# Kernel tuning notes

Measured on AMD Instinct MI355X. Metric: run time of the kernel, lower is better.

Reference implementation:

```python
import jax, jax.numpy as jnp
import numpy as np

C = 256
R = 2
HEADS = 8
HEAD_DIM = C // HEADS
SCALE = HEAD_DIM ** -0.5
EPS = 1e-5


def setup_inputs() -> dict:
    key = jax.random.key(0)
    ks = jax.random.split(key, 7)
    x = jax.random.normal(ks[0], (8, C, 64, 64), dtype=jnp.float32)
    # qkv 1x1 conv weight [3C, C], no bias
    w_qkv = jax.random.normal(ks[1], (3 * C, C), dtype=jnp.float32) * (C ** -0.5)
    # depthwise ConvTranspose2d(C, C, k=r, stride=r, groups=C): weight [C, r, r], bias [C]
    w_lp = jax.random.normal(ks[2], (C, R, R), dtype=jnp.float32) * 0.5
    b_lp = jax.random.normal(ks[3], (C,), dtype=jnp.float32) * 0.01
    # GroupNorm(1, C) affine params
    gamma = jnp.ones((C,), dtype=jnp.float32)
    beta = jnp.zeros((C,), dtype=jnp.float32)
    # proj 1x1 conv weight [C, C], no bias
    w_proj = jax.random.normal(ks[4], (C, C), dtype=jnp.float32) * (C ** -0.5)
    return {"x": x, "w_qkv": w_qkv, "w_lp": w_lp, "b_lp": b_lp,
            "gamma": gamma, "beta": beta, "w_proj": w_proj}


def reference(x, w_qkv, w_lp, b_lp, gamma, beta, w_proj):
    # sparse_sampler: AvgPool2d(kernel=1, stride=r) == strided subsampling
    xs = x[:, :, ::R, ::R]                      # [B, C, H, W]
    B, _, H, W = xs.shape
    N = H * W
    # qkv 1x1 conv -> [B, 3C, N] -> [B, heads, 3*head_dim, N]
    qkv = jnp.einsum('oc,bcn->bon', w_qkv, xs.reshape(B, C, N))
    qkv = qkv.reshape(B, HEADS, 3 * HEAD_DIM, N)
    q, k, v = jnp.split(qkv, 3, axis=2)         # each [B, h, d, N]
    # attn[b,h,i,j] = softmax_j( (q^T k)[i,j] * scale )
    attn = jax.nn.softmax(jnp.einsum('bhdi,bhdj->bhij', q, k) * SCALE, axis=-1)
    # out[b,h,d,i] = sum_j v[b,h,d,j] attn[b,h,i,j]
    out = jnp.einsum('bhdj,bhij->bhdi', v, attn).reshape(B, C, H, W)
    # depthwise ConvTranspose2d kernel=r stride=r (non-overlapping): broadcast each
    # pixel into an r x r block weighted by the per-channel kernel, plus bias.
    up = jnp.einsum('bchw,cpq->bchpwq', out, w_lp).reshape(B, C, H * R, W * R)
    up = up + b_lp[None, :, None, None]
    # GroupNorm with 1 group: normalize over (C, H, W) per sample
    mu = jnp.mean(up, axis=(1, 2, 3), keepdims=True)
    var = jnp.var(up, axis=(1, 2, 3), keepdims=True)
    normed = (up - mu) * jax.lax.rsqrt(var + EPS)
    normed = normed * gamma[None, :, None, None] + beta[None, :, None, None]
    # proj 1x1 conv
    Bo, _, Ho, Wo = normed.shape
    y = jnp.einsum('oc,bcn->bon', w_proj, normed.reshape(Bo, C, Ho * Wo))
    return y.reshape(Bo, C, Ho, Wo)
```

## Files before the change

kernel.cpp:

```cpp
#include <hip/hip_runtime.h>
#include <hip/hip_bf16.h>

#define ATT_SCALE_L2E 0.2550322540f

typedef __attribute__((ext_vector_type(8))) short bf16x8;
typedef __attribute__((ext_vector_type(4))) short bf16x4;
typedef __attribute__((ext_vector_type(4))) float f32x4;
typedef __attribute__((ext_vector_type(16))) float f32x16;
typedef __attribute__((ext_vector_type(4))) int i32x4;

#define MFMA16(a, b, c) __builtin_amdgcn_mfma_f32_16x16x32_bf16(a, b, c, 0, 0, 0)
#define MFMA32(a, b, c) __builtin_amdgcn_mfma_f32_32x32x16_bf16(a, b, c, 0, 0, 0)

__device__ inline short f2b(float f) {
    return __builtin_bit_cast(short, __float2bfloat16(f));
}

__device__ inline bf16x8 cat4(bf16x4 a, bf16x4 b) {
    bf16x8 r;
    r[0] = a[0]; r[1] = a[1]; r[2] = a[2]; r[3] = a[3];
    r[4] = b[0]; r[5] = b[1]; r[6] = b[2]; r[7] = b[3];
    return r;
}

__device__ inline int cvt_pk(float a, float b) {
    int r;
    asm("v_cvt_pk_bf16_f32 %0, %1, %2" : "=v"(r) : "v"(a), "v"(b));
    return r;
}

__global__ __launch_bounds__(256) void wconv_k(const float* __restrict__ w,
                                               short* __restrict__ wb) {
    int i0 = (blockIdx.x * 256 + threadIdx.x) * 8;
    float4 lo = *(const float4*)(w + i0);
    float4 hi = *(const float4*)(w + i0 + 4);
    bf16x8 o;
    o[0] = f2b(lo.x); o[1] = f2b(lo.y); o[2] = f2b(lo.z); o[3] = f2b(lo.w);
    o[4] = f2b(hi.x); o[5] = f2b(hi.y); o[6] = f2b(hi.z); o[7] = f2b(hi.w);
    *(bf16x8*)(wb + i0) = o;
}

__global__ __launch_bounds__(256) void xt_k(const float* __restrict__ x,
                                            short* __restrict__ xt) {
    int b = blockIdx.y;
    int t = threadIdx.x;
    int n = blockIdx.x * 32 + (t >> 3);
    const float* xb = x + (size_t)b * 1048576 + (n >> 5) * 128 + (n & 31) * 2;
    short* dst = xt + ((size_t)b * 1024 + n) * 256;
#pragma unroll
    for (int it = 0; it < 4; ++it) {
        int c = (t & 7) * 8 + it * 64;
        bf16x8 o;
#pragma unroll
        for (int j = 0; j < 8; ++j) o[j] = f2b(xb[(size_t)(c + j) * 4096]);
        *(bf16x8*)(dst + c) = o;
    }
}

__global__ __launch_bounds__(256) void qkv_k(const short* __restrict__ wb,
                                             const short* __restrict__ xt,
                                             short* __restrict__ qt,
                                             short* __restrict__ kt,
                                             short* __restrict__ vvr) {
    int b = blockIdx.x;
    int ntile = blockIdx.y * 128;
    int otile = blockIdx.z * 64;
    int t = threadIdx.x;
    int w = t >> 6, l = t & 63, g = l >> 4, li = l & 15;
    int oh = (w & 1) * 32, mh = (w >> 1) * 64;
    int o_base = otile + oh;
    int head = o_base / 96;
    int role = (o_base >> 5) % 3;
    size_t bh = (size_t)b * 8 + head;

    const short* arow = wb + (size_t)o_base * 256;
    const short* brow = xt + ((size_t)b * 1024 + ntile + mh) * 256;

    f32x4 zero = {0.f, 0.f, 0.f, 0.f};
    f32x4 acc[2][4];
#pragma unroll
    for (int og = 0; og < 2; ++og)
#pragma unroll
        for (int mg = 0; mg < 4; ++mg) acc[og][mg] = zero;

#pragma unroll
    for (int kc = 0; kc < 256; kc += 32) {
        bf16x8 af[2], bf_[4];
#pragma unroll
        for (int og = 0; og < 2; ++og)
            af[og] = *(const bf16x8*)(arow + (size_t)(og * 16 + li) * 256 + kc + 8 * g);
#pragma unroll
        for (int mg = 0; mg < 4; ++mg)
            bf_[mg] = *(const bf16x8*)(brow + (size_t)(mg * 16 + li) * 256 + kc + 8 * g);
#pragma unroll
        for (int og = 0; og < 2; ++og)
#pragma unroll
            for (int mg = 0; mg < 4; ++mg)
                acc[og][mg] = MFMA16(af[og], bf_[mg], acc[og][mg]);
    }

    __shared__ short Tl[4][32][64];
    short (*Tw)[64] = Tl[w];
    float sc = (role == 0) ? ATT_SCALE_L2E : 1.f;

#pragma unroll
    for (int og = 0; og < 2; ++og)
#pragma unroll
        for (int mg = 0; mg < 4; ++mg)
#pragma unroll
            for (int r = 0; r < 4; ++r) {
                int op = og * 16 + 4 * g + r;
                int qp = (op >> 3) & 3;
                Tw[op][(mg * 16 + li) ^ (qp << 4)] = f2b(acc[og][mg][r] * sc);
            }
    __syncthreads();

    if (role == 2) {
#pragma unroll
        for (int it = 0; it < 8; ++it) {
            int s = it * 64 + l;
            int d = s & 31;
            int n_rel = (s >> 5) * 4;
            int n = ntile + mh + n_rel;
            int jb = n >> 5;
            int q = (n & 31) >> 3;
            int hi2 = (n & 7) >> 2;
            int q2 = (d >> 3) & 3;
            bf16x4 vo = *(const bf16x4*)&Tw[d][n_rel ^ (q2 << 4)];
            *(bf16x4*)(vvr + (size_t)bh * 32768 +
                       ((((size_t)jb * 4 + q) * 2 + hi2) * 32 + d) * 4) = vo;
        }
    } else {
        short* dst = (role == 0) ? qt : kt;
#pragma unroll
        for (int it = 0; it < 4; ++it) {
            int s = it * 64 + l;
            int dq = (l & 3) * 8;
            int n = s >> 2;
            int q2 = dq >> 3;
            bf16x8 vo;
#pragma unroll
            for (int j = 0; j < 8; ++j)
                vo[j] = Tw[dq + j][n ^ (q2 << 4)];
            *(bf16x8*)(dst + ((size_t)bh * 1024 + ntile + mh + n) * 32 + dq) = vo;
        }
    }
}

__global__ __launch_bounds__(256) void attn_k(const short* __restrict__ qt,
                                              const short* __restrict__ kt,
                                              const short* __restrict__ vvr,
                                              float* __restrict__ ao2) {
    int bh = blockIdx.x;
    int b = bh >> 3, h = bh & 7;
    int w = threadIdx.x >> 6, l = threadIdx.x & 63;
    int il = l & 31, hi = l >> 5;
    int ibase = blockIdx.y * 128 + w * 32;

    const short* qtb = qt + (size_t)bh * 32768;
    const short* ktb = kt + (size_t)bh * 32768;
    const short* vbase = vvr + (size_t)bh * 32768 + (hi * 32 + il) * 4;

    bf16x8 qf0 = *(const bf16x8*)(qtb + (size_t)(ibase + il) * 32 + 8 * hi);
    bf16x8 qf1 = *(const bf16x8*)(qtb + (size_t)(ibase + il) * 32 + 16 + 8 * hi);

    f32x16 zero16 = {0.f,0.f,0.f,0.f,0.f,0.f,0.f,0.f,0.f,0.f,0.f,0.f,0.f,0.f,0.f,0.f};
    f32x16 oacc = zero16;
    float lrun = 0.f;

#pragma unroll 2
    for (int jb = 0; jb < 32; ++jb) {
        int j0 = jb * 32;
        bf16x8 kf0 = *(const bf16x8*)(ktb + (size_t)(j0 + il) * 32 + 8 * hi);
        bf16x8 kf1 = *(const bf16x8*)(ktb + (size_t)(j0 + il) * 32 + 16 + 8 * hi);
        f32x16 s = MFMA32(kf0, qf0, zero16);
        s = MFMA32(kf1, qf1, s);

        float p[16];
#pragma unroll
        for (int r = 0; r < 16; ++r) {
            p[r] = exp2f(s[r]);
            lrun += p[r];
        }

        i32x4 fa, fb;
        fa[0] = cvt_pk(p[0], p[1]);   fa[1] = cvt_pk(p[2], p[3]);
        fa[2] = cvt_pk(p[4], p[5]);   fa[3] = cvt_pk(p[6], p[7]);
        fb[0] = cvt_pk(p[8], p[9]);   fb[1] = cvt_pk(p[10], p[11]);
        fb[2] = cvt_pk(p[12], p[13]); fb[3] = cvt_pk(p[14], p[15]);
        bf16x8 pfa = __builtin_bit_cast(bf16x8, fa);
        bf16x8 pfb = __builtin_bit_cast(bf16x8, fb);

        bf16x8 vfa = cat4(*(const bf16x4*)(vbase + (size_t)(jb * 4 + 0) * 256),
                          *(const bf16x4*)(vbase + (size_t)(jb * 4 + 1) * 256));
        bf16x8 vfb = cat4(*(const bf16x4*)(vbase + (size_t)(jb * 4 + 2) * 256),
                          *(const bf16x4*)(vbase + (size_t)(jb * 4 + 3) * 256));

        oacc = MFMA32(vfa, pfa, oacc);
        oacc = MFMA32(vfb, pfb, oacc);
    }

    float tot = lrun + __shfl_xor(lrun, 32);
    float inv = 1.f / tot;

    float* base = ao2 + ((size_t)(b * 256 + h * 32)) * 1024 + ibase + il;
#pragma unroll
    for (int r = 0; r < 16; ++r) {
        int d = (r & 3) + 8 * (r >> 2) + 4 * hi;
        base[(size_t)d * 1024] = oacc[r] * inv;
    }
}

__global__ __launch_bounds__(64) void psum_k(const float* __restrict__ ao2,
                                             float* __restrict__ p1,
                                             float* __restrict__ p2) {
    int row = blockIdx.x;
    const float* base = ao2 + (size_t)row * 1024;
    int l = threadIdx.x;
    float s = 0.f, q = 0.f;
#pragma unroll
    for (int t = 0; t < 4; ++t) {
        float4 v = *(const float4*)(base + l * 4 + t * 256);
        s += v.x + v.y + v.z + v.w;
        q += v.x * v.x + v.y * v.y + v.z * v.z + v.w * v.w;
    }
#pragma unroll
    for (int o = 1; o < 64; o <<= 1) {
        s += __shfl_xor(s, o);
        q += __shfl_xor(q, o);
    }
    if (l == 0) { p1[row] = s; p2[row] = q; }
}

__global__ __launch_bounds__(256) void stats_k(const float* __restrict__ p1,
                                               const float* __restrict__ p2,
                                               const float* __restrict__ wlp,
                                               const float* __restrict__ blp,
                                               float* __restrict__ stats) {
    int b = blockIdx.x, c = threadIdx.x;
    float s = p1[b * 256 + c];
    float q = p2[b * 256 + c];
    float w0 = wlp[c * 4], w1 = wlp[c * 4 + 1], w2 = wlp[c * 4 + 2], w3 = wlp[c * 4 + 3];
    float S1 = w0 + w1 + w2 + w3, S2 = w0 * w0 + w1 * w1 + w2 * w2 + w3 * w3;
    float bl = blp[c];
    float su = S1 * s + 4096.f * bl;
    float sq = S2 * q + 2.f * bl * S1 * s + 4096.f * bl * bl;
    __shared__ float rs_[256], rq_[256];
    rs_[c] = su; rq_[c] = sq;
    __syncthreads();
    for (int o = 128; o > 0; o >>= 1) {
        if (c < o) { rs_[c] += rs_[c + o]; rq_[c] += rq_[c + o]; }
        __syncthreads();
    }
    if (c == 0) {
        const float N = 1048576.f;
        float mu = rs_[0] / N;
        float var = rq_[0] / N - mu * mu;
        stats[b] = mu;
        stats[8 + b] = rsqrtf(var + 1e-5f);
    }
}

__global__ __launch_bounds__(256) void proj_k(const float* __restrict__ ao2,
                                              const float* __restrict__ wp,
                                              const float* __restrict__ wlp,
                                              const float* __restrict__ blp,
                                              const float* __restrict__ gamma,
                                              const float* __restrict__ beta,
                                              const float* __restrict__ stats,
                                              float* __restrict__ y) {
    int b = blockIdx.x;
    int mt = blockIdx.y;
    int otile = blockIdx.z * 64;
    float mu = stats[b], rs = stats[8 + b];

    __shared__ short As[64][40];
    __shared__ short Bs[128][40];

    int t = threadIdx.x;
    int w = t >> 6, l = t & 63, g = l >> 4, li = l & 15;
    int oh = (w >> 1) * 32, mh = (w & 1) * 64;

    f32x4 zero = {0.f, 0.f, 0.f, 0.f};
    f32x4 acc[2][4];
#pragma unroll
    for (int og = 0; og < 2; ++og)
#pragma unroll
        for (int mg = 0; mg < 4; ++mg) acc[og][mg] = zero;

    int so = t >> 2, sc = (t & 3) * 8;
    int bc = t & 31, bm = (t >> 5) * 16;
    int p = t >> 7;
    int wbase = bm & 63;

    for (int kc = 0; kc < 256; kc += 32) {
        const float* wrow = wp + (size_t)(otile + so) * 256 + kc + sc;
#pragma unroll
        for (int j = 0; j < 8; ++j) As[so][sc + j] = f2b(wrow[j]);
        int c = kc + bc;
        float Ac = gamma[c] * rs;
        float Dc = Ac * (blp[c] - mu) + beta[c];
        float w0 = Ac * wlp[c * 4 + p * 2 + 0];
        float w1 = Ac * wlp[c * 4 + p * 2 + 1];
        const float* arow = ao2 + ((size_t)(b * 256 + c)) * 1024 + mt * 32 + (wbase >> 1);
        float4 a0 = *(const float4*)arow;
        float4 a1 = *(const float4*)(arow + 4);
        float av[8] = {a0.x, a0.y, a0.z, a0.w, a1.x, a1.y, a1.z, a1.w};
#pragma unroll
        for (int k = 0; k < 8; ++k) {
            Bs[bm + 2 * k    ][bc] = f2b(w0 * av[k] + Dc);
            Bs[bm + 2 * k + 1][bc] = f2b(w1 * av[k] + Dc);
        }
        __syncthreads();
        bf16x8 af[2], bf_[4];
#pragma unroll
        for (int og = 0; og < 2; ++og) af[og] = *(const bf16x8*)&As[oh + og * 16 + li][8 * g];
#pragma unroll
        for (int mg = 0; mg < 4; ++mg) bf_[mg] = *(const bf16x8*)&Bs[mh + mg * 16 + li][8 * g];
#pragma unroll
        for (int og = 0; og < 2; ++og)
#pragma unroll
            for (int mg = 0; mg < 4; ++mg) acc[og][mg] = MFMA16(af[og], bf_[mg], acc[og][mg]);
        __syncthreads();
    }

#pragma unroll
    for (int og = 0; og < 2; ++og) {
        int o = otile + oh + og * 16 + 4 * g;
#pragma unroll
        for (int mg = 0; mg < 4; ++mg) {
            int m = mt * 128 + mh + mg * 16 + li;
            float* yp = y + ((size_t)b * 256 + o) * 4096 + m;
#pragma unroll
            for (int r = 0; r < 4; ++r) yp[(size_t)r * 4096] = acc[og][mg][r];
        }
    }
}

extern "C" void kernel_launch(void* const* d_in, const int* in_sizes, int n_in,
                              void* d_out, int out_size, void* d_ws, size_t ws_size,
                              hipStream_t stream) {
    const float* x      = (const float*)d_in[0];
    const float* w_qkv  = (const float*)d_in[1];
    const float* w_lp   = (const float*)d_in[2];
    const float* b_lp   = (const float*)d_in[3];
    const float* gamma  = (const float*)d_in[4];
    const float* beta   = (const float*)d_in[5];
    const float* w_proj = (const float*)d_in[6];
    float* y = (float*)d_out;

    short* qt   = (short*)d_out;
    short* kt   = qt + 2097152;
    short* vvr  = kt + 2097152;
    short* xt   = vvr + 2097152;
    short* wbuf = xt + 2097152;

    float* ao2   = (float*)d_ws;
    float* p1    = ao2 + 2097152;
    float* p2    = p1 + 2048;
    float* stats = p2 + 2048;

    wconv_k<<<96, 256, 0, stream>>>(w_qkv, wbuf);
    xt_k<<<dim3(32, 8), 256, 0, stream>>>(x, xt);
    qkv_k<<<dim3(8, 8, 12), 256, 0, stream>>>(wbuf, xt, qt, kt, vvr);
    attn_k<<<dim3(64, 8), 256, 0, stream>>>(qt, kt, vvr, ao2);
    psum_k<<<2048, 64, 0, stream>>>(ao2, p1, p2);
    stats_k<<<8, 256, 0, stream>>>(p1, p2, w_lp, b_lp, stats);
    proj_k<<<dim3(8, 32, 4), 256, 0, stream>>>(ao2, w_proj, w_lp, b_lp, gamma, beta, stats, y);
}
```

Measured before the change: 86.07 us.

## Swizzle K/V into fragment-contiguous layout and double-buffer loads in attention

The QKV kernel now writes K and V in a per-32-key-block layout where each lane's MFMA fragment is 8 contiguous bf16s, so the attention kernel can use single 16-byte coalesced loads instead of strided or split 8-byte loads. The attention loop is fully unrolled with register double-buffering of the next block's K/V fragments to hide global load latency. It also raises wave priority around MFMAs and splits the row-sum accumulation into four chains to shorten dependencies. The cost is higher register pressure and a larger unrolled loop body.

```diff
diff --git a/kernel.cpp b/kernel.cpp
--- a/kernel.cpp
+++ b/kernel.cpp
@@ -14,13 +14,6 @@
 
 __device__ inline short f2b(float f) {
     return __builtin_bit_cast(short, __float2bfloat16(f));
-}
-
-__device__ inline bf16x8 cat4(bf16x4 a, bf16x4 b) {
-    bf16x8 r;
-    r[0] = a[0]; r[1] = a[1]; r[2] = a[2]; r[3] = a[3];
-    r[4] = b[0]; r[5] = b[1]; r[6] = b[2]; r[7] = b[3];
-    return r;
 }
 
 __device__ inline int cvt_pk(float a, float b) {
@@ -60,7 +53,7 @@
 __global__ __launch_bounds__(256) void qkv_k(const short* __restrict__ wb,
                                              const short* __restrict__ xt,
                                              short* __restrict__ qt,
-                                             short* __restrict__ kt,
+                                             short* __restrict__ ktr,
                                              short* __restrict__ vvr) {
     int b = blockIdx.x;
     int ntile = blockIdx.y * 128;
@@ -115,23 +108,7 @@
             }
     __syncthreads();
 
-    if (role == 2) {
-#pragma unroll
-        for (int it = 0; it < 8; ++it) {
-            int s = it * 64 + l;
-            int d = s & 31;
-            int n_rel = (s >> 5) * 4;
-            int n = ntile + mh + n_rel;
-            int jb = n >> 5;
-            int q = (n & 31) >> 3;
-            int hi2 = (n & 7) >> 2;
-            int q2 = (d >> 3) & 3;
-            bf16x4 vo = *(const bf16x4*)&Tw[d][n_rel ^ (q2 << 4)];
-            *(bf16x4*)(vvr + (size_t)bh * 32768 +
-                       ((((size_t)jb * 4 + q) * 2 + hi2) * 32 + d) * 4) = vo;
-        }
-    } else {
-        short* dst = (role == 0) ? qt : kt;
+    if (role == 0) {
 #pragma unroll
         for (int it = 0; it < 4; ++it) {
             int s = it * 64 + l;
@@ -142,13 +119,49 @@
 #pragma unroll
             for (int j = 0; j < 8; ++j)
                 vo[j] = Tw[dq + j][n ^ (q2 << 4)];
-            *(bf16x8*)(dst + ((size_t)bh * 1024 + ntile + mh + n) * 32 + dq) = vo;
+            *(bf16x8*)(qt + ((size_t)bh * 1024 + ntile + mh + n) * 32 + dq) = vo;
+        }
+    } else if (role == 1) {
+        int base_jb = (ntile + mh) >> 5;
+#pragma unroll
+        for (int it = 0; it < 4; ++it) {
+            int s = it * 64 + l;
+            int il2 = s & 31;
+            int combo = (s >> 5) & 3;
+            int jbr = s >> 7;
+            int dq = combo * 8;
+            int n_rel = jbr * 32 + il2;
+            bf16x8 vo;
+#pragma unroll
+            for (int j = 0; j < 8; ++j)
+                vo[j] = Tw[dq + j][n_rel ^ (combo << 4)];
+            *(bf16x8*)(ktr + (size_t)bh * 32768 +
+                       (size_t)(base_jb + jbr) * 1024 + combo * 256 + il2 * 8) = vo;
+        }
+    } else {
+        int base_jb = (ntile + mh) >> 5;
+#pragma unroll
+        for (int it = 0; it < 4; ++it) {
+            int s = it * 64 + l;
+            int il2 = s & 31;
+            int combo = (s >> 5) & 3;
+            int jbr = s >> 7;
+            int pan = combo >> 1, hi2 = combo & 1;
+            int q2 = (il2 >> 3) & 3;
+            int bn = jbr * 32 + pan * 16 + 4 * hi2;
+            bf16x8 vo;
+#pragma unroll
+            for (int j = 0; j < 4; ++j) vo[j] = Tw[il2][(bn + j) ^ (q2 << 4)];
+#pragma unroll
+            for (int j = 0; j < 4; ++j) vo[4 + j] = Tw[il2][(bn + 8 + j) ^ (q2 << 4)];
+            *(bf16x8*)(vvr + (size_t)bh * 32768 +
+                       (size_t)(base_jb + jbr) * 1024 + combo * 256 + il2 * 8) = vo;
         }
     }
 }
 
 __global__ __launch_bounds__(256) void attn_k(const short* __restrict__ qt,
-                                              const short* __restrict__ kt,
+                                              const short* __restrict__ ktr,
                                               const short* __restrict__ vvr,
                                               float* __restrict__ ao2) {
     int bh = blockIdx.x;
@@ -158,30 +171,47 @@
     int ibase = blockIdx.y * 128 + w * 32;
 
     const short* qtb = qt + (size_t)bh * 32768;
-    const short* ktb = kt + (size_t)bh * 32768;
-    const short* vbase = vvr + (size_t)bh * 32768 + (hi * 32 + il) * 4;
+    const short* kbase = ktr + (size_t)bh * 32768 + hi * 256 + il * 8;
+    const short* vbase = vvr + (size_t)bh * 32768 + hi * 256 + il * 8;
 
     bf16x8 qf0 = *(const bf16x8*)(qtb + (size_t)(ibase + il) * 32 + 8 * hi);
     bf16x8 qf1 = *(const bf16x8*)(qtb + (size_t)(ibase + il) * 32 + 16 + 8 * hi);
 
     f32x16 zero16 = {0.f,0.f,0.f,0.f,0.f,0.f,0.f,0.f,0.f,0.f,0.f,0.f,0.f,0.f,0.f,0.f};
     f32x16 oacc = zero16;
-    float lrun = 0.f;
-
-#pragma unroll 2
+    float lr0 = 0.f, lr1 = 0.f, lr2 = 0.f, lr3 = 0.f;
+
+    bf16x8 kf0[2], kf1[2], vfa[2], vfb[2];
+    kf0[0] = *(const bf16x8*)(kbase);
+    kf1[0] = *(const bf16x8*)(kbase + 512);
+    vfa[0] = *(const bf16x8*)(vbase);
+    vfb[0] = *(const bf16x8*)(vbase + 512);
+
+#pragma unroll
     for (int jb = 0; jb < 32; ++jb) {
-        int j0 = jb * 32;
-        bf16x8 kf0 = *(const bf16x8*)(ktb + (size_t)(j0 + il) * 32 + 8 * hi);
-        bf16x8 kf1 = *(const bf16x8*)(ktb + (size_t)(j0 + il) * 32 + 16 + 8 * hi);
-        f32x16 s = MFMA32(kf0, qf0, zero16);
-        s = MFMA32(kf1, qf1, s);
+        int cur = jb & 1;
+        if (jb < 31) {
+            int nx = cur ^ 1;
+            const short* kp = kbase + (size_t)(jb + 1) * 1024;
+            const short* vp = vbase + (size_t)(jb + 1) * 1024;
+            kf0[nx] = *(const bf16x8*)(kp);
+            kf1[nx] = *(const bf16x8*)(kp + 512);
+            vfa[nx] = *(const bf16x8*)(vp);
+            vfb[nx] = *(const bf16x8*)(vp + 512);
+        }
+
+        __builtin_amdgcn_s_setprio(1);
+        f32x16 s = MFMA32(kf0[cur], qf0, zero16);
+        s = MFMA32(kf1[cur], qf1, s);
+        __builtin_amdgcn_s_setprio(0);
 
         float p[16];
 #pragma unroll
-        for (int r = 0; r < 16; ++r) {
-            p[r] = exp2f(s[r]);
-            lrun += p[r];
-        }
+        for (int r = 0; r < 16; ++r) p[r] = exp2f(s[r]);
+        lr0 += p[0] + p[4] + p[8]  + p[12];
+        lr1 += p[1] + p[5] + p[9]  + p[13];
+        lr2 += p[2] + p[6] + p[10] + p[14];
+        lr3 += p[3] + p[7] + p[11] + p[15];
 
         i32x4 fa, fb;
         fa[0] = cvt_pk(p[0], p[1]);   fa[1] = cvt_pk(p[2], p[3]);
@@ -191,15 +221,13 @@
         bf16x8 pfa = __builtin_bit_cast(bf16x8, fa);
         bf16x8 pfb = __builtin_bit_cast(bf16x8, fb);
 
-        bf16x8 vfa = cat4(*(const bf16x4*)(vbase + (size_t)(jb * 4 + 0) * 256),
-                          *(const bf16x4*)(vbase + (size_t)(jb * 4 + 1) * 256));
-        bf16x8 vfb = cat4(*(const bf16x4*)(vbase + (size_t)(jb * 4 + 2) * 256),
-                          *(const bf16x4*)(vbase + (size_t)(jb * 4 + 3) * 256));
-
-        oacc = MFMA32(vfa, pfa, oacc);
-        oacc = MFMA32(vfb, pfb, oacc);
-    }
-
+        __builtin_amdgcn_s_setprio(1);
+        oacc = MFMA32(vfa[cur], pfa, oacc);
+        oacc = MFMA32(vfb[cur], pfb, oacc);
+        __builtin_amdgcn_s_setprio(0);
+    }
+
+    float lrun = (lr0 + lr1) + (lr2 + lr3);
     float tot = lrun + __shfl_xor(lrun, 32);
     float inv = 1.f / tot;
 
@@ -350,8 +378,8 @@
     float* y = (float*)d_out;
 
     short* qt   = (short*)d_out;
-    short* kt   = qt + 2097152;
-    short* vvr  = kt + 2097152;
+    short* ktr  = qt + 2097152;
+    short* vvr  = ktr + 2097152;
     short* xt   = vvr + 2097152;
     short* wbuf = xt + 2097152;
 
@@ -362,8 +390,8 @@
 
     wconv_k<<<96, 256, 0, stream>>>(w_qkv, wbuf);
     xt_k<<<dim3(32, 8), 256, 0, stream>>>(x, xt);
-    qkv_k<<<dim3(8, 8, 12), 256, 0, stream>>>(wbuf, xt, qt, kt, vvr);
-    attn_k<<<dim3(64, 8), 256, 0, stream>>>(qt, kt, vvr, ao2);
+    qkv_k<<<dim3(8, 8, 12), 256, 0, stream>>>(wbuf, xt, qt, ktr, vvr);
+    attn_k<<<dim3(64, 8), 256, 0, stream>>>(qt, ktr, vvr, ao2);
     psum_k<<<2048, 64, 0, stream>>>(ao2, p1, p2);
     stats_k<<<8, 256, 0, stream>>>(p1, p2, w_lp, b_lp, stats);
     proj_k<<<dim3(8, 32, 4), 256, 0, stream>>>(ao2, w_proj, w_lp, b_lp, gamma, beta, stats, y);
```

Result: slower. 108.9 us (+26.5%).
